# Kernel tuning notes

Hardware: AMD Instinct MI355X
Metric: run time of the kernel (lower is better)

Reference implementation:

```python
import jax, jax.numpy as jnp
import numpy as np

# Dimensions
B, S, F, PATCH, D, H, NL, DFF, HOR = 512, 336, 12, 6, 512, 8, 6, 2048, 24
NP = S // PATCH        # 56 temporal patches
DH = D // H            # head dim = 64
EPS = 1e-5


def layer_norm(x, g, b):
    m = jnp.mean(x, axis=-1, keepdims=True)
    v = jnp.mean(jnp.square(x - m), axis=-1, keepdims=True)
    return (x - m) * jax.lax.rsqrt(v + EPS) * g + b


def alibi_bias(n_heads, n):
    # slopes = 2^(-8h/H), h = 1..H (standard ALiBi, H power of 2)
    slopes = 2.0 ** (-8.0 * jnp.arange(1, n_heads + 1, dtype=jnp.float32) / n_heads)
    pos = jnp.arange(n, dtype=jnp.float32)
    dist = jnp.abs(pos[:, None] - pos[None, :])         # [n, n]
    return -slopes[:, None, None] * dist                # [H, n, n]


def setup_inputs() -> dict:
    key = jax.random.key(0)
    ks = jax.random.split(key, 16)
    g = lambda k, shape: jax.random.normal(k, shape, dtype=jnp.float32) * 0.02
    return {
        "x": jax.random.normal(ks[0], (B, S, F), dtype=jnp.float32),
        "patch_W": g(ks[1], (PATCH * F, D)),
        "patch_b": jnp.zeros((D,), jnp.float32),
        "pos": g(ks[2], (NP, D)),
        "ln1_g": jnp.ones((NL, D), jnp.float32),
        "ln1_b": jnp.zeros((NL, D), jnp.float32),
        "Wq": g(ks[3], (NL, D, D)), "bq": jnp.zeros((NL, D), jnp.float32),
        "Wk": g(ks[4], (NL, D, D)), "bk": jnp.zeros((NL, D), jnp.float32),
        "Wv": g(ks[5], (NL, D, D)), "bv": jnp.zeros((NL, D), jnp.float32),
        "Wo": g(ks[6], (NL, D, D)), "bo": jnp.zeros((NL, D), jnp.float32),
        "ln2_g": jnp.ones((NL, D), jnp.float32),
        "ln2_b": jnp.zeros((NL, D), jnp.float32),
        "W1": g(ks[7], (NL, D, DFF)), "b1": jnp.zeros((NL, DFF), jnp.float32),
        "W2": g(ks[8], (NL, DFF, D)), "b2": jnp.zeros((NL, D), jnp.float32),
        "fn_g": jnp.ones((D,), jnp.float32),
        "fn_b": jnp.zeros((D,), jnp.float32),
        "head_W": g(ks[9], (D, HOR)),
        "head_b": jnp.zeros((HOR,), jnp.float32),
    }


def reference(x, patch_W, patch_b, pos, ln1_g, ln1_b, Wq, bq, Wk, bk, Wv, bv,
              Wo, bo, ln2_g, ln2_b, W1, b1, W2, b2, fn_g, fn_b, head_W, head_b):
    # Temporal patch embedding: (B,S,F) -> (B,NP,PATCH*F) -> Linear -> +pos
    h = x.reshape(B, NP, PATCH * F) @ patch_W + patch_b + pos  # [B, NP, D]
    bias = alibi_bias(H, NP)                                   # [H, NP, NP]
    scale = 1.0 / np.sqrt(DH).astype(np.float32)
    for l in range(NL):
        # Pre-LN multi-head attention with ALiBi temporal decay bias
        hn = layer_norm(h, ln1_g[l], ln1_b[l])
        q = (hn @ Wq[l] + bq[l]).reshape(B, NP, H, DH)
        k = (hn @ Wk[l] + bk[l]).reshape(B, NP, H, DH)
        v = (hn @ Wv[l] + bv[l]).reshape(B, NP, H, DH)
        sc = jnp.einsum('bqhd,bkhd->bhqk', q, k) * scale + bias[None]
        a = jax.nn.softmax(sc, axis=-1)
        o = jnp.einsum('bhqk,bkhd->bqhd', a, v).reshape(B, NP, D)
        h = h + (o @ Wo[l] + bo[l])
        # Pre-LN feedforward
        hn2 = layer_norm(h, ln2_g[l], ln2_b[l])
        h = h + (jax.nn.gelu(hn2 @ W1[l] + b1[l]) @ W2[l] + b2[l])
    pooled = jnp.mean(h, axis=1)                               # [B, D]
    out = layer_norm(pooled, fn_g, fn_b) @ head_W + head_b     # [B, HOR]
    return out
```

## Files before the change

### kernel.cpp

```cpp
#include <hip/hip_runtime.h>
#include <hip/hip_bf16.h>
#include <math.h>

#define D_      512
#define NPATCH  56
#define DFF_    2048
#define NLAYER  6
#define HEADS   8
#define DH_     64
#define HOR_    24
#define BATCH_  512
#define NTOK_   (BATCH_ * NPATCH)
#define KPAD    96

typedef __hip_bfloat16 bf16;
typedef __bf16 bf16x8 __attribute__((ext_vector_type(8)));
typedef float  f32x4  __attribute__((ext_vector_type(4)));

__device__ __forceinline__ void gload_lds16(const void* g, void* lds) {
    __builtin_amdgcn_global_load_lds(
        (const __attribute__((address_space(1))) unsigned int*)g,
        (__attribute__((address_space(3))) unsigned int*)lds, 16, 0, 0);
}

__device__ __forceinline__ float block_sum256(float v) {
    __shared__ float sm[4];
    const int lane = threadIdx.x & 63;
    const int w    = threadIdx.x >> 6;
    #pragma unroll
    for (int o = 32; o > 0; o >>= 1) v += __shfl_down(v, o);
    __syncthreads();
    if (lane == 0) sm[w] = v;
    __syncthreads();
    return sm[0] + sm[1] + sm[2] + sm[3];
}

__device__ __forceinline__ float gelu_fast(float xg) {
    const float e = __expf(1.5957691216057308f * (xg + 0.044715f * xg * xg * xg));
    return xg - xg * __builtin_amdgcn_rcpf(1.f + e);
}

__global__ __launch_bounds__(256) void transpose_bf16_k(
    const float* __restrict__ in, bf16* __restrict__ out, int R, int C,
    size_t in_ls, size_t out_ls)
{
    __shared__ float t[32][33];
    in  += (size_t)blockIdx.z * in_ls;
    out += (size_t)blockIdx.z * out_ls;
    const int c0 = blockIdx.x * 32, r0 = blockIdx.y * 32;
    const int x = threadIdx.x & 31, y = threadIdx.x >> 5;
    #pragma unroll
    for (int i = 0; i < 4; i++)
        t[y + i * 8][x] = in[(size_t)(r0 + y + i * 8) * C + c0 + x];
    __syncthreads();
    #pragma unroll
    for (int i = 0; i < 4; i++)
        out[(size_t)(c0 + y + i * 8) * R + r0 + x] = __float2bfloat16(t[x][y + i * 8]);
}

__global__ __launch_bounds__(256) void pwt_k(
    const float* __restrict__ W, bf16* __restrict__ out)
{
    const int idx = blockIdx.x * 256 + threadIdx.x;
    if (idx >= D_ * KPAD) return;
    const int n = idx / KPAD, kk = idx % KPAD;
    out[idx] = (kk < 72) ? __float2bfloat16(W[kk * D_ + n]) : __float2bfloat16(0.f);
}

__global__ __launch_bounds__(256) void xpad_k(
    const float* __restrict__ x, bf16* __restrict__ out)
{
    const size_t idx = (size_t)blockIdx.x * 256 + threadIdx.x;
    if (idx >= (size_t)NTOK_ * KPAD) return;
    const size_t row = idx / KPAD;
    const int kk = (int)(idx - row * KPAD);
    out[idx] = (kk < 72) ? __float2bfloat16(x[row * 72 + kk]) : __float2bfloat16(0.f);
}

__global__ __launch_bounds__(256) void bqkv_k(
    const float* __restrict__ bq, const float* __restrict__ bk,
    const float* __restrict__ bv, float* __restrict__ o)
{
    const int idx = blockIdx.x * 256 + threadIdx.x;
    if (idx >= NLAYER * 3 * D_) return;
    const int l = idx / (3 * D_), n = idx % (3 * D_);
    float v;
    if      (n < D_)     v = bq[l * D_ + n];
    else if (n < 2 * D_) v = bk[l * D_ + n - D_];
    else                 v = bv[l * D_ + n - 2 * D_];
    o[idx] = v;
}

__global__ __launch_bounds__(256) void layernorm_bf16_k(
    const float* __restrict__ x, const float* __restrict__ g,
    const float* __restrict__ b, bf16* __restrict__ y)
{
    const int w = threadIdx.x >> 6, lane = threadIdx.x & 63;
    const size_t row = (size_t)blockIdx.x * 4 + w;
    const float* xr = x + row * D_ + lane * 8;
    const float4 a0 = *(const float4*)xr;
    const float4 a1 = *(const float4*)(xr + 4);
    float s = a0.x + a0.y + a0.z + a0.w + a1.x + a1.y + a1.z + a1.w;
    #pragma unroll
    for (int o = 32; o > 0; o >>= 1) s += __shfl_xor(s, o);
    const float mean = s * (1.f / 512.f);
    float d[8] = {a0.x - mean, a0.y - mean, a0.z - mean, a0.w - mean,
                  a1.x - mean, a1.y - mean, a1.z - mean, a1.w - mean};
    float v = 0.f;
    #pragma unroll
    for (int i = 0; i < 8; i++) v += d[i] * d[i];
    #pragma unroll
    for (int o = 32; o > 0; o >>= 1) v += __shfl_xor(v, o);
    const float rstd = rsqrtf(v * (1.f / 512.f) + 1e-5f);
    const float4 g0 = *(const float4*)(g + lane * 8);
    const float4 g1 = *(const float4*)(g + lane * 8 + 4);
    const float4 b0 = *(const float4*)(b + lane * 8);
    const float4 b1 = *(const float4*)(b + lane * 8 + 4);
    const float gg[8] = {g0.x, g0.y, g0.z, g0.w, g1.x, g1.y, g1.z, g1.w};
    const float bb[8] = {b0.x, b0.y, b0.z, b0.w, b1.x, b1.y, b1.z, b1.w};
    bf16x8 o8;
    #pragma unroll
    for (int i = 0; i < 8; i++) o8[i] = (__bf16)(d[i] * rstd * gg[i] + bb[i]);
    *(bf16x8*)((__bf16*)y + row * D_ + lane * 8) = o8;
}

template<bool OUT_BF16, bool GELU, bool RESID, bool POS, bool QKVSPLIT>
__global__ __launch_bounds__(512, 2) void gemm_bf16_k(
    const bf16* __restrict__ A, const bf16* __restrict__ Bt,
    const float* __restrict__ bias, const float* __restrict__ resid,
    const float* __restrict__ pos, void* __restrict__ Cp,
    bf16* __restrict__ vt, int M, int N, int K, int nx)
{
    __shared__ __align__(16) bf16 As[2][256 * 32];
    __shared__ __align__(16) bf16 Bs[2][256 * 32];
    const int tid  = threadIdx.x;
    const int wid  = tid >> 6;
    const int lane = tid & 63;

    const int nwg = gridDim.x;
    const int q8 = nwg >> 3, r8 = nwg & 7;
    const int xcd = blockIdx.x & 7, idx8 = blockIdx.x >> 3;
    const int swz = (xcd < r8 ? xcd * (q8 + 1) : r8 * (q8 + 1) + (xcd - r8) * q8) + idx8;
    const int n0 = (swz % nx) * 256;
    const int m0 = (swz / nx) * 256;
    const int wr = wid >> 2;
    const int wn = wid & 3;

    f32x4 acc[8][4];
    #pragma unroll
    for (int m = 0; m < 8; m++)
        #pragma unroll
        for (int n = 0; n < 4; n++) acc[m][n] = f32x4{0.f, 0.f, 0.f, 0.f};

    const int srow = lane >> 2;
    const int schunk = ((lane & 3) ^ ((lane >> 3) & 3)) * 8;
    const bf16* gA = A  + (size_t)(m0 + wid * 32 + srow) * K + schunk;
    const bf16* gB = Bt + (size_t)(n0 + wid * 32 + srow) * K + schunk;
    const size_t k16 = (size_t)16 * K;
    const int s0 = (wid * 2 + 0) * 512, s1 = (wid * 2 + 1) * 512;

    const int fr = lane & 15;
    const int qg = lane >> 4;
    const int roff = fr * 32 + ((qg ^ ((fr >> 1) & 3)) * 8);

    const int nt = K >> 5;
    gload_lds16(gA,       &As[0][s0]);
    gload_lds16(gA + k16, &As[0][s1]);
    gload_lds16(gB,       &Bs[0][s0]);
    gload_lds16(gB + k16, &Bs[0][s1]);
    asm volatile("s_waitcnt vmcnt(0)" ::: "memory");
    __builtin_amdgcn_s_barrier();

    int cur = 0;
    for (int t = 0; t < nt; t++) {
        bf16x8 bg[4], af[4];
        #pragma unroll
        for (int n = 0; n < 4; n++) bg[n] = *(const bf16x8*)&Bs[cur][(wn * 4 + n) * 512 + roff];
        #pragma unroll
        for (int m = 0; m < 4; m++) af[m] = *(const bf16x8*)&As[cur][(wr * 8 + m) * 512 + roff];
        if (t + 1 < nt) {
            const int kn = (t + 1) << 5;
            gload_lds16(gA + kn,       &As[cur ^ 1][s0]);
            gload_lds16(gA + kn + k16, &As[cur ^ 1][s1]);
            gload_lds16(gB + kn,       &Bs[cur ^ 1][s0]);
            gload_lds16(gB + kn + k16, &Bs[cur ^ 1][s1]);
        }
        __builtin_amdgcn_s_barrier();
        asm volatile("s_waitcnt lgkmcnt(0)" ::: "memory");
        __builtin_amdgcn_sched_barrier(0);
        __builtin_amdgcn_s_setprio(1);
        #pragma unroll
        for (int m = 0; m < 4; m++)
            #pragma unroll
            for (int n = 0; n < 4; n++)
                acc[m][n] = __builtin_amdgcn_mfma_f32_16x16x32_bf16(af[m], bg[n], acc[m][n], 0, 0, 0);
        __builtin_amdgcn_s_setprio(0);
        __builtin_amdgcn_s_barrier();
        #pragma unroll
        for (int m = 0; m < 4; m++) af[m] = *(const bf16x8*)&As[cur][(wr * 8 + 4 + m) * 512 + roff];
        __builtin_amdgcn_s_barrier();
        asm volatile("s_waitcnt lgkmcnt(0)" ::: "memory");
        __builtin_amdgcn_sched_barrier(0);
        __builtin_amdgcn_s_setprio(1);
        #pragma unroll
        for (int m = 0; m < 4; m++)
            #pragma unroll
            for (int n = 0; n < 4; n++)
                acc[4 + m][n] = __builtin_amdgcn_mfma_f32_16x16x32_bf16(af[m], bg[n], acc[4 + m][n], 0, 0, 0);
        __builtin_amdgcn_s_setprio(0);
        asm volatile("s_waitcnt vmcnt(0)" ::: "memory");
        __builtin_amdgcn_s_barrier();
        cur ^= 1;
    }

    const int rq = qg * 4;
    #pragma unroll
    for (int m = 0; m < 8; m++) {
        #pragma unroll
        for (int n = 0; n < 4; n++) {
            const int col = n0 + wn * 64 + n * 16 + fr;
            const float bcol = bias[col];
            #pragma unroll
            for (int j = 0; j < 4; j++) {
                const int row = m0 + wr * 128 + m * 16 + rq + j;
                float c = acc[m][n][j] + bcol;
                if (GELU)  c = gelu_fast(c);
                if (RESID) c += resid[(size_t)row * N + col];
                if (POS)   c += pos[(size_t)(row % NPATCH) * D_ + col];
                if (QKVSPLIT) {
                    if (col < 1024) {
                        ((bf16*)Cp)[(size_t)row * 1024 + col] = __float2bfloat16(c);
                    } else {
                        const int c2 = col - 1024, hh = c2 >> 6, dd = c2 & 63;
                        const int bb = row / NPATCH, pp = row - bb * NPATCH;
                        vt[(((size_t)bb * 8 + hh) * 64 + dd) * 64 + pp] = __float2bfloat16(c);
                    }
                } else if (OUT_BF16) {
                    ((bf16*)Cp)[(size_t)row * N + col] = __float2bfloat16(c);
                } else {
                    ((float*)Cp)[(size_t)row * N + col] = c;
                }
            }
        }
    }
}

__global__ __launch_bounds__(256) void attn_mfma_k(
    const bf16* __restrict__ qk, const bf16* __restrict__ vt,
    bf16* __restrict__ ao)
{
    __shared__ __align__(16) bf16 St[4][64 * 72];
    const int tid  = threadIdx.x;
    const int w    = tid >> 6, lane = tid & 63;
    const int bh   = blockIdx.x * 4 + w;
    const int b    = bh >> 3, hh = bh & 7;
    const int fr   = lane & 15;
    const int qg   = lane >> 4;
    const int kc   = qg * 8;

    const bf16* Qb = qk + (size_t)b * NPATCH * 1024 + hh * 64;
    const bf16* Kb = Qb + 512;
    const bf16* Vb = vt + (size_t)bh * 4096;

    bf16x8 qf[4][2], kf[4][2];
    #pragma unroll
    for (int m = 0; m < 4; m++)
        #pragma unroll
        for (int ks = 0; ks < 2; ks++) {
            qf[m][ks] = *(const bf16x8*)&Qb[(size_t)(m * 16 + fr) * 1024 + ks * 32 + kc];
            kf[m][ks] = *(const bf16x8*)&Kb[(size_t)(m * 16 + fr) * 1024 + ks * 32 + kc];
        }

    f32x4 acc[4][4];
    #pragma unroll
    for (int m = 0; m < 4; m++)
        #pragma unroll
        for (int n = 0; n < 4; n++) acc[m][n] = f32x4{0.f, 0.f, 0.f, 0.f};
    #pragma unroll
    for (int ks = 0; ks < 2; ks++)
        #pragma unroll
        for (int m = 0; m < 4; m++)
            #pragma unroll
            for (int n = 0; n < 4; n++)
                acc[m][n] = __builtin_amdgcn_mfma_f32_16x16x32_bf16(qf[m][ks], kf[n][ks], acc[m][n], 0, 0, 0);

    bf16x8 vf[4][2];
    #pragma unroll
    for (int n = 0; n < 4; n++)
        #pragma unroll
        for (int ks = 0; ks < 2; ks++)
            vf[n][ks] = *(const bf16x8*)&Vb[(size_t)(n * 16 + fr) * 64 + ks * 32 + kc];

    const float slope = exp2f(-(float)(hh + 1));
    bf16* Sw = St[w];
    #pragma unroll
    for (int m = 0; m < 4; m++) {
        #pragma unroll
        for (int j = 0; j < 4; j++) {
            const int r = m * 16 + qg * 4 + j;
            float s[4];
            #pragma unroll
            for (int n = 0; n < 4; n++) {
                const int col = n * 16 + fr;
                float sv = acc[m][n][j] * 0.125f - slope * fabsf((float)(r - col));
                s[n] = (col >= NPATCH) ? -1e30f : sv;
            }
            float mx = fmaxf(fmaxf(s[0], s[1]), fmaxf(s[2], s[3]));
            mx = fmaxf(mx, __shfl_xor(mx, 1));
            mx = fmaxf(mx, __shfl_xor(mx, 2));
            mx = fmaxf(mx, __shfl_xor(mx, 4));
            mx = fmaxf(mx, __shfl_xor(mx, 8));
            float p[4], sum = 0.f;
            #pragma unroll
            for (int n = 0; n < 4; n++) { p[n] = __expf(s[n] - mx); sum += p[n]; }
            sum += __shfl_xor(sum, 1);
            sum += __shfl_xor(sum, 2);
            sum += __shfl_xor(sum, 4);
            sum += __shfl_xor(sum, 8);
            const float inv = 1.f / sum;
            #pragma unroll
            for (int n = 0; n < 4; n++)
                Sw[r * 72 + n * 16 + fr] = __float2bfloat16(p[n] * inv);
        }
    }

    #pragma unroll
    for (int m = 0; m < 4; m++)
        #pragma unroll
        for (int n = 0; n < 4; n++) acc[m][n] = f32x4{0.f, 0.f, 0.f, 0.f};
    #pragma unroll
    for (int m = 0; m < 4; m++)
        #pragma unroll
        for (int ks = 0; ks < 2; ks++) {
            const bf16x8 pf = *(const bf16x8*)&Sw[(m * 16 + fr) * 72 + ks * 32 + kc];
            #pragma unroll
            for (int n = 0; n < 4; n++)
                acc[m][n] = __builtin_amdgcn_mfma_f32_16x16x32_bf16(pf, vf[n][ks], acc[m][n], 0, 0, 0);
        }

    bf16* Ob = ao + (size_t)b * NPATCH * 512 + hh * 64;
    #pragma unroll
    for (int m = 0; m < 4; m++)
        #pragma unroll
        for (int j = 0; j < 4; j++) {
            const int r = m * 16 + qg * 4 + j;
            if (r < NPATCH)
                #pragma unroll
                for (int n = 0; n < 4; n++)
                    Ob[(size_t)r * 512 + n * 16 + fr] = __float2bfloat16(acc[m][n][j]);
        }
}

__global__ __launch_bounds__(256) void meanpool_k(
    const float* __restrict__ h, float* __restrict__ pooled)
{
    const int b = blockIdx.x;
    for (int d = threadIdx.x; d < D_; d += 256) {
        float acc = 0.f;
        #pragma unroll
        for (int p = 0; p < NPATCH; p++)
            acc += h[(size_t)b * NPATCH * D_ + (size_t)p * D_ + d];
        pooled[(size_t)b * D_ + d] = acc * (1.f / (float)NPATCH);
    }
}

__global__ __launch_bounds__(256) void head_k(
    const float* __restrict__ pooled, const float* __restrict__ g,
    const float* __restrict__ bb, const float* __restrict__ hW,
    const float* __restrict__ hb, float* __restrict__ out)
{
    const int b = blockIdx.x;
    __shared__ float row[D_];
    const int tid = threadIdx.x;
    const float v0 = pooled[(size_t)b * D_ + tid];
    const float v1 = pooled[(size_t)b * D_ + tid + 256];
    const float mean = block_sum256(v0 + v1) * (1.f / 512.f);
    const float d0 = v0 - mean, d1 = v1 - mean;
    const float var = block_sum256(d0 * d0 + d1 * d1) * (1.f / 512.f);
    const float rstd = rsqrtf(var + 1e-5f);
    row[tid]       = d0 * rstd * g[tid]       + bb[tid];
    row[tid + 256] = d1 * rstd * g[tid + 256] + bb[tid + 256];
    __syncthreads();
    if (tid < HOR_) {
        float acc = hb[tid];
        for (int kk = 0; kk < D_; kk++) acc = fmaf(row[kk], hW[kk * HOR_ + tid], acc);
        out[(size_t)b * HOR_ + tid] = acc;
    }
}

extern "C" void kernel_launch(void* const* d_in, const int* in_sizes, int n_in,
                              void* d_out, int out_size, void* d_ws, size_t ws_size,
                              hipStream_t stream)
{
    const float* x       = (const float*)d_in[0];
    const float* patch_W = (const float*)d_in[1];
    const float* patch_b = (const float*)d_in[2];
    const float* pos     = (const float*)d_in[3];
    const float* ln1_g   = (const float*)d_in[4];
    const float* ln1_b   = (const float*)d_in[5];
    const float* Wq      = (const float*)d_in[6];
    const float* bq      = (const float*)d_in[7];
    const float* Wk      = (const float*)d_in[8];
    const float* bk      = (const float*)d_in[9];
    const float* Wv      = (const float*)d_in[10];
    const float* bv      = (const float*)d_in[11];
    const float* Wo      = (const float*)d_in[12];
    const float* bo      = (const float*)d_in[13];
    const float* ln2_g   = (const float*)d_in[14];
    const float* ln2_b   = (const float*)d_in[15];
    const float* W1      = (const float*)d_in[16];
    const float* b1      = (const float*)d_in[17];
    const float* W2      = (const float*)d_in[18];
    const float* b2      = (const float*)d_in[19];
    const float* fn_g    = (const float*)d_in[20];
    const float* fn_b    = (const float*)d_in[21];
    const float* head_W  = (const float*)d_in[22];
    const float* head_b  = (const float*)d_in[23];
    float* out = (float*)d_out;

    const size_t WELEM  = (size_t)D_ * D_;
    const size_t WFELEM = (size_t)D_ * DFF_;
    bf16* wqkvt = (bf16*)d_ws;
    bf16* wot   = wqkvt + (size_t)NLAYER * 3 * WELEM;
    bf16* w1t   = wot   + (size_t)NLAYER * WELEM;
    bf16* w2t   = w1t   + (size_t)NLAYER * WFELEM;
    bf16* pwt   = w2t   + (size_t)NLAYER * WFELEM;
    float* bqkv = (float*)(pwt + (size_t)D_ * KPAD);
    bf16* xpad  = (bf16*)(bqkv + NLAYER * 3 * D_);
    char* wend  = (char*)(xpad + (size_t)NTOK_ * KPAD);
    const size_t FIXED = (size_t)(wend - (char*)d_ws);

    int BC = 32;
    for (int cand = BATCH_; cand >= 32; cand >>= 1) {
        const size_t need = FIXED + (size_t)cand * (56 * 6144 + 65536 + 2048);
        if (need <= ws_size) { BC = cand; break; }
    }
    const int nChunks = BATCH_ / BC;
    const int CT = BC * NPATCH;
    const size_t TD = (size_t)CT * D_;

    float* h    = (float*)wend;
    bf16*  hn   = (bf16*)(h + TD);
    bf16*  qk   = hn + TD;
    bf16*  ao   = qk + (size_t)CT * 1024;
    bf16*  vt   = ao + TD;
    bf16*  mid  = qk;
    float* pooled = (float*)(vt + (size_t)BC * 8 * 64 * 64);

    transpose_bf16_k<<<dim3(16, 16, NLAYER), 256, 0, stream>>>(
        Wq, wqkvt,                 D_, D_, WELEM, 3 * WELEM);
    transpose_bf16_k<<<dim3(16, 16, NLAYER), 256, 0, stream>>>(
        Wk, wqkvt + WELEM,         D_, D_, WELEM, 3 * WELEM);
    transpose_bf16_k<<<dim3(16, 16, NLAYER), 256, 0, stream>>>(
        Wv, wqkvt + 2 * WELEM,     D_, D_, WELEM, 3 * WELEM);
    transpose_bf16_k<<<dim3(16, 16, NLAYER), 256, 0, stream>>>(
        Wo, wot,                   D_, D_, WELEM, WELEM);
    transpose_bf16_k<<<dim3(64, 16, NLAYER), 256, 0, stream>>>(
        W1, w1t,                   D_, DFF_, WFELEM, WFELEM);
    transpose_bf16_k<<<dim3(16, 64, NLAYER), 256, 0, stream>>>(
        W2, w2t,                   DFF_, D_, WFELEM, WFELEM);
    pwt_k<<<(D_ * KPAD + 255) / 256, 256, 0, stream>>>(patch_W, pwt);
    bqkv_k<<<(NLAYER * 3 * D_ + 255) / 256, 256, 0, stream>>>(bq, bk, bv, bqkv);
    xpad_k<<<((size_t)NTOK_ * KPAD + 255) / 256, 256, 0, stream>>>(x, xpad);

    const int mt  = CT / 256;
    const int g1n = 2 * mt;
    const int gqn = 6 * mt;
    const int g2n = 8 * mt;

    for (int c = 0; c < nChunks; c++) {
        const size_t tok0 = (size_t)c * CT;

        gemm_bf16_k<false, false, false, true, false><<<g1n, 512, 0, stream>>>(
            xpad + tok0 * KPAD, pwt, patch_b, nullptr, pos, h, nullptr,
            CT, D_, KPAD, 2);

        for (int l = 0; l < NLAYER; l++) {
            layernorm_bf16_k<<<CT / 4, 256, 0, stream>>>(h, ln1_g + l * D_, ln1_b + l * D_, hn);
            gemm_bf16_k<true, false, false, false, true><<<gqn, 512, 0, stream>>>(
                hn, wqkvt + (size_t)l * 3 * WELEM, bqkv + l * 3 * D_, nullptr, nullptr,
                qk, vt, CT, 3 * D_, D_, 6);
            attn_mfma_k<<<BC * 2, 256, 0, stream>>>(qk, vt, ao);
            gemm_bf16_k<false, false, true, false, false><<<g1n, 512, 0, stream>>>(
                ao, wot + (size_t)l * WELEM, bo + l * D_, h, nullptr, h, nullptr,
                CT, D_, D_, 2);
            layernorm_bf16_k<<<CT / 4, 256, 0, stream>>>(h, ln2_g + l * D_, ln2_b + l * D_, hn);
            gemm_bf16_k<true, true, false, false, false><<<g2n, 512, 0, stream>>>(
                hn, w1t + (size_t)l * WFELEM, b1 + l * DFF_, nullptr, nullptr,
                mid, nullptr, CT, DFF_, D_, 8);
            gemm_bf16_k<false, false, true, false, false><<<g1n, 512, 0, stream>>>(
                mid, w2t + (size_t)l * WFELEM, b2 + l * D_, h, nullptr, h, nullptr,
                CT, D_, DFF_, 2);
        }

        meanpool_k<<<BC, 256, 0, stream>>>(h, pooled);
        head_k<<<BC, 256, 0, stream>>>(pooled, fn_g, fn_b, head_W, head_b,
                                       out + (size_t)c * BC * HOR_);
    }
}
```

Before: 2.404 ms.

## Double the GEMM K-tile to 64 and stagger sub-tile prefetches between MFMA phases

The bf16 GEMM main loop now stages a 64-wide K slice per iteration, held as two 32-wide sub-tiles per buffer. The next tile's A and B halves are issued one at a time between the four MFMA phases, with partial vmcnt waits, so global-to-LDS traffic is spread across the compute rather than issued in one burst. This halves the number of loop iterations and thins out the barrier structure. The cost is double the LDS footprint, 128KB per block, which likely prevents the two resident blocks per CU that the launch bounds request, and KPAD rises to 128 so the patch-embedding K is a multiple of 64.

```diff
diff --git a/kernel.cpp b/kernel.cpp
--- a/kernel.cpp
+++ b/kernel.cpp
@@ -11,7 +11,7 @@
 #define HOR_    24
 #define BATCH_  512
 #define NTOK_   (BATCH_ * NPATCH)
-#define KPAD    96
+#define KPAD    128
 
 typedef __hip_bfloat16 bf16;
 typedef __bf16 bf16x8 __attribute__((ext_vector_type(8)));
@@ -131,8 +131,8 @@
     const float* __restrict__ pos, void* __restrict__ Cp,
     bf16* __restrict__ vt, int M, int N, int K, int nx)
 {
-    __shared__ __align__(16) bf16 As[2][256 * 32];
-    __shared__ __align__(16) bf16 Bs[2][256 * 32];
+    __shared__ __align__(16) bf16 As[2][256 * 64];
+    __shared__ __align__(16) bf16 Bs[2][256 * 64];
     const int tid  = threadIdx.x;
     const int wid  = tid >> 6;
     const int lane = tid & 63;
@@ -163,29 +163,31 @@
     const int qg = lane >> 4;
     const int roff = fr * 32 + ((qg ^ ((fr >> 1) & 3)) * 8);
 
-    const int nt = K >> 5;
-    gload_lds16(gA,       &As[0][s0]);
-    gload_lds16(gA + k16, &As[0][s1]);
-    gload_lds16(gB,       &Bs[0][s0]);
-    gload_lds16(gB + k16, &Bs[0][s1]);
+    const int nt = K >> 6;
+
+    #define STAGE_A(buf, kt, sub)  do { const bf16* _s = gA + ((kt) << 6) + (sub) * 32; \
+        gload_lds16(_s,       &As[buf][(sub) * 8192 + s0]);                              \
+        gload_lds16(_s + k16, &As[buf][(sub) * 8192 + s1]); } while (0)
+    #define STAGE_B(buf, kt, sub)  do { const bf16* _s = gB + ((kt) << 6) + (sub) * 32; \
+        gload_lds16(_s,       &Bs[buf][(sub) * 8192 + s0]);                              \
+        gload_lds16(_s + k16, &Bs[buf][(sub) * 8192 + s1]); } while (0)
+
+    STAGE_A(0, 0, 0); STAGE_A(0, 0, 1);
+    STAGE_B(0, 0, 0); STAGE_B(0, 0, 1);
     asm volatile("s_waitcnt vmcnt(0)" ::: "memory");
     __builtin_amdgcn_s_barrier();
 
     int cur = 0;
     for (int t = 0; t < nt; t++) {
-        bf16x8 bg[4], af[4];
+        const bool pre = (t + 1 < nt);
+        bf16x8 af[4], bg[4];
+        asm volatile("s_waitcnt vmcnt(2)" ::: "memory");
+        __builtin_amdgcn_s_barrier();
+        if (pre) STAGE_A(cur ^ 1, t + 1, 0);
         #pragma unroll
         for (int n = 0; n < 4; n++) bg[n] = *(const bf16x8*)&Bs[cur][(wn * 4 + n) * 512 + roff];
         #pragma unroll
         for (int m = 0; m < 4; m++) af[m] = *(const bf16x8*)&As[cur][(wr * 8 + m) * 512 + roff];
-        if (t + 1 < nt) {
-            const int kn = (t + 1) << 5;
-            gload_lds16(gA + kn,       &As[cur ^ 1][s0]);
-            gload_lds16(gA + kn + k16, &As[cur ^ 1][s1]);
-            gload_lds16(gB + kn,       &Bs[cur ^ 1][s0]);
-            gload_lds16(gB + kn + k16, &Bs[cur ^ 1][s1]);
-        }
-        __builtin_amdgcn_s_barrier();
         asm volatile("s_waitcnt lgkmcnt(0)" ::: "memory");
         __builtin_amdgcn_sched_barrier(0);
         __builtin_amdgcn_s_setprio(1);
@@ -196,9 +198,9 @@
                 acc[m][n] = __builtin_amdgcn_mfma_f32_16x16x32_bf16(af[m], bg[n], acc[m][n], 0, 0, 0);
         __builtin_amdgcn_s_setprio(0);
         __builtin_amdgcn_s_barrier();
+        if (pre) STAGE_A(cur ^ 1, t + 1, 1);
         #pragma unroll
         for (int m = 0; m < 4; m++) af[m] = *(const bf16x8*)&As[cur][(wr * 8 + 4 + m) * 512 + roff];
-        __builtin_amdgcn_s_barrier();
         asm volatile("s_waitcnt lgkmcnt(0)" ::: "memory");
         __builtin_amdgcn_sched_barrier(0);
         __builtin_amdgcn_s_setprio(1);
@@ -208,10 +210,39 @@
             for (int n = 0; n < 4; n++)
                 acc[4 + m][n] = __builtin_amdgcn_mfma_f32_16x16x32_bf16(af[m], bg[n], acc[4 + m][n], 0, 0, 0);
         __builtin_amdgcn_s_setprio(0);
-        asm volatile("s_waitcnt vmcnt(0)" ::: "memory");
+        asm volatile("s_waitcnt vmcnt(4)" ::: "memory");
         __builtin_amdgcn_s_barrier();
+        if (pre) STAGE_B(cur ^ 1, t + 1, 0);
+        #pragma unroll
+        for (int n = 0; n < 4; n++) bg[n] = *(const bf16x8*)&Bs[cur][8192 + (wn * 4 + n) * 512 + roff];
+        #pragma unroll
+        for (int m = 0; m < 4; m++) af[m] = *(const bf16x8*)&As[cur][8192 + (wr * 8 + m) * 512 + roff];
+        asm volatile("s_waitcnt lgkmcnt(0)" ::: "memory");
+        __builtin_amdgcn_sched_barrier(0);
+        __builtin_amdgcn_s_setprio(1);
+        #pragma unroll
+        for (int m = 0; m < 4; m++)
+            #pragma unroll
+            for (int n = 0; n < 4; n++)
+                acc[m][n] = __builtin_amdgcn_mfma_f32_16x16x32_bf16(af[m], bg[n], acc[m][n], 0, 0, 0);
+        __builtin_amdgcn_s_setprio(0);
+        __builtin_amdgcn_s_barrier();
+        if (pre) STAGE_B(cur ^ 1, t + 1, 1);
+        #pragma unroll
+        for (int m = 0; m < 4; m++) af[m] = *(const bf16x8*)&As[cur][8192 + (wr * 8 + 4 + m) * 512 + roff];
+        asm volatile("s_waitcnt lgkmcnt(0)" ::: "memory");
+        __builtin_amdgcn_sched_barrier(0);
+        __builtin_amdgcn_s_setprio(1);
+        #pragma unroll
+        for (int m = 0; m < 4; m++)
+            #pragma unroll
+            for (int n = 0; n < 4; n++)
+                acc[4 + m][n] = __builtin_amdgcn_mfma_f32_16x16x32_bf16(af[m], bg[n], acc[4 + m][n], 0, 0, 0);
+        __builtin_amdgcn_s_setprio(0);
         cur ^= 1;
     }
+    #undef STAGE_A
+    #undef STAGE_B
 
     const int rq = qg * 4;
     #pragma unroll
```

Result: slower. 2.693 ms (+12.0%).
